# Optimization experiments

Measured on AMD Instinct MI355X. Metric: run time of the kernel, lower is better.

Reference implementation:

```python
import jax, jax.numpy as jnp
import numpy as np


def setup_inputs() -> dict:
    key = jax.random.key(0)
    k1, k2 = jax.random.split(key)
    # x: [B, D, H, W, C] 3D latent grid, C == embedding_dim
    x = jax.random.normal(k1, (4, 32, 32, 16, 256), dtype=jnp.float32)
    # codebook stored as (embedding_dim, num_embeddings) like the TF variable
    embeddings = jax.random.uniform(k2, (256, 4096), dtype=jnp.float32)
    return {"x": x, "embeddings": embeddings}


def reference(x, embeddings):
    # Inference-mode forward of VectorQuantizer.call (training=False).
    D, K = embeddings.shape  # (embedding_dim, num_embeddings)
    flat = x.reshape(-1, D)  # [N, D]
    # squared L2 distances: ||z||^2 + ||e||^2 - 2 z.e  -> [N, K]
    sim = flat @ embeddings
    dist = (jnp.sum(flat * flat, axis=1, keepdims=True)
            + jnp.sum(embeddings * embeddings, axis=0)
            - 2.0 * sim)
    idx = jnp.argmin(dist, axis=1)  # [N]
    # nearest-codebook lookup (gather codebook columns)
    quantized = jnp.take(embeddings.T, idx, axis=0).reshape(x.shape)
    # perplexity from code usage histogram (avoids materializing [N,K] one-hot)
    n = flat.shape[0]
    counts = jnp.zeros((K,), dtype=jnp.float32).at[idx].add(1.0)
    avg_probs = counts / n
    perplexity = jnp.exp(-jnp.sum(avg_probs * jnp.log(avg_probs + 1e-10)))
    return quantized, perplexity
```

## Files before the change

kernel.cpp:

```cpp
#include <hip/hip_runtime.h>
#include <hip/hip_bf16.h>

#define NROWS 65536
#define DIM   256
#define KCB   4096
#define CHUNK 32
#define NCH   (KCB / CHUNK)
#define NBUF  4
#define BUFB  16384
#define NENH_BASE (NBUF * BUFB)

typedef __attribute__((ext_vector_type(8))) short bf16x8;
typedef __attribute__((ext_vector_type(4))) float f32x4;

#define WAITV0 asm volatile("s_waitcnt vmcnt(0)" ::: "memory")
#define WAITV4 asm volatile("s_waitcnt vmcnt(4)" ::: "memory")
#define WAITV8 asm volatile("s_waitcnt vmcnt(8)" ::: "memory")

__device__ inline short f2bf(float f) {
    __hip_bfloat16 h = __float2bfloat16(f);
    return *reinterpret_cast<short*>(&h);
}

__global__ void prep_transpose(const float* __restrict__ E,
                               float* __restrict__ ET32,
                               ushort* __restrict__ ETbf)
{
    __shared__ float tile[64][65];
    const int kb = blockIdx.x * 64;
    const int db = blockIdx.y * 64;
    const int lo = threadIdx.x & 63;
    const int hi = threadIdx.x >> 6;

#pragma unroll
    for (int i = 0; i < 16; ++i) {
        int d = i * 4 + hi;
        tile[lo][d] = E[(size_t)(db + d) * KCB + kb + lo];
    }
    __syncthreads();
#pragma unroll
    for (int i = 0; i < 16; ++i) {
        int k = i * 4 + hi;
        float v = tile[k][lo];
        size_t off = (size_t)(kb + k) * DIM + db + lo;
        ET32[off] = v;
        ETbf[off] = (ushort)f2bf(v);
    }
}

__global__ void prep_enorm(const float* __restrict__ E, float* __restrict__ nenh)
{
    int k = blockIdx.x * 256 + threadIdx.x;
    float s = 0.0f;
#pragma unroll 8
    for (int d = 0; d < DIM; ++d) {
        float v = E[(size_t)d * KCB + k];
        s = fmaf(v, v, s);
    }
    nenh[k] = -0.5f * s;
}

__shared__ char lds_raw[NBUF * BUFB + 16384];

template <int BUF>
__device__ __forceinline__ void stage_chunk(
    const char* __restrict__ etb, const int (&soff)[4], int wave, int ct)
{
    const char* base = etb + (size_t)ct * (CHUNK * 512);
#pragma unroll
    for (int j = 0; j < 4; ++j) {
        __builtin_amdgcn_global_load_lds(
            (const __attribute__((address_space(1))) unsigned*)(base + soff[j]),
            (__attribute__((address_space(3))) unsigned*)
                (lds_raw + BUF * BUFB + wave * 4096 + j * 1024),
            16, 0, 0);
    }
}

template <int BUF, int TC>
__device__ __forceinline__ void read_batch(
    const int (&boffB)[8], int nhbyte, bf16x8 (&bfr)[8], float& nh)
{
#pragma unroll
    for (int kc = 0; kc < 8; ++kc)
        bfr[kc] = *(const bf16x8*)(lds_raw + BUF * BUFB + TC * 8192 + boffB[kc]);
    nh = *(const float*)(lds_raw + NENH_BASE + nhbyte);
}

__device__ __forceinline__ void mfma_cluster(
    const bf16x8 (&afrag)[2][8], const bf16x8 (&bfr)[8], float nh,
    float (&best)[2][4], int (&bidx)[2][4], int col)
{
    f32x4 acc0 = {nh, nh, nh, nh};
    f32x4 acc1 = {nh, nh, nh, nh};
    __builtin_amdgcn_s_setprio(1);
#pragma unroll
    for (int kc = 0; kc < 8; ++kc) {
        acc0 = __builtin_amdgcn_mfma_f32_16x16x32_bf16(afrag[0][kc], bfr[kc], acc0, 0, 0, 0);
        acc1 = __builtin_amdgcn_mfma_f32_16x16x32_bf16(afrag[1][kc], bfr[kc], acc1, 0, 0, 0);
    }
    __builtin_amdgcn_s_setprio(0);
#pragma unroll
    for (int r = 0; r < 4; ++r) {
        float s0 = acc0[r];
        bool g0 = s0 > best[0][r];
        bidx[0][r] = g0 ? col : bidx[0][r];
        best[0][r] = fmaxf(best[0][r], s0);
        float s1 = acc1[r];
        bool g1 = s1 > best[1][r];
        bidx[1][r] = g1 ? col : bidx[1][r];
        best[1][r] = fmaxf(best[1][r], s1);
    }
}

template <int BUF, int WN, bool STG, bool RA>
__device__ __forceinline__ void chunk_step(
    const char* __restrict__ etb, const int (&soff)[4], int wave, int ct,
    const int (&boffB)[8], int l15,
    const bf16x8 (&afrag)[2][8],
    bf16x8 (&bA)[8], bf16x8 (&bB)[8], float& nhA, float& nhB,
    float (&best)[2][4], int (&bidx)[2][4])
{
    if constexpr (WN == 4) { WAITV4; } else { WAITV0; }
    __builtin_amdgcn_s_barrier();
    __builtin_amdgcn_sched_barrier(0);
    if constexpr (STG) stage_chunk<(BUF + 3) & 3>(etb, soff, wave, ct + 3);
    read_batch<BUF, 1>(boffB, ct * 128 + 64 + l15 * 4, bB, nhB);
    mfma_cluster(afrag, bA, nhA, best, bidx, ct * CHUNK + l15);
    if constexpr (RA)
        read_batch<(BUF + 1) & 3, 0>(boffB, (ct + 1) * 128 + l15 * 4, bA, nhA);
    mfma_cluster(afrag, bB, nhB, best, bidx, ct * CHUNK + 16 + l15);
}

__global__ __launch_bounds__(256, 2)
void vq_argmin(const float* __restrict__ X,
               const ushort* __restrict__ ETbf,
               const float* __restrict__ nenh,
               int* __restrict__ idxout)
{
    const int tid  = threadIdx.x;
    const int lane = tid & 63;
    const int wave = tid >> 6;
    const int l15  = lane & 15;
    const int g    = lane >> 4;
    const int m    = l15 & 7;
    const long rowbase = (long)blockIdx.x * 128 + wave * 32;
    const char* etb = (const char*)ETbf;

    bf16x8 afrag[2][8];
#pragma unroll
    for (int rt = 0; rt < 2; ++rt) {
        const float* xr = X + (rowbase + rt * 16 + l15) * DIM;
#pragma unroll
        for (int kc = 0; kc < 8; ++kc) {
            int k0 = g * 64 + kc * 8;
            float4 v0 = *(const float4*)(xr + k0);
            float4 v1 = *(const float4*)(xr + k0 + 4);
            bf16x8 f;
            f[0] = f2bf(v0.x); f[1] = f2bf(v0.y);
            f[2] = f2bf(v0.z); f[3] = f2bf(v0.w);
            f[4] = f2bf(v1.x); f[5] = f2bf(v1.y);
            f[6] = f2bf(v1.z); f[7] = f2bf(v1.w);
            afrag[rt][kc] = f;
        }
    }

    int soff[4];
#pragma unroll
    for (int j = 0; j < 4; ++j) {
        const int o    = wave * 4096 + j * 1024 + lane * 16;
        const int col0 = o >> 9;
        const int cph  = (o >> 4) & 31;
        soff[j] = (col0 << 9) + ((cph ^ (col0 & 7)) << 4);
    }

    int boffB[8];
#pragma unroll
    for (int kc = 0; kc < 8; ++kc)
        boffB[kc] = l15 * 512 + ((((g << 3) + kc) ^ m) << 4);

#pragma unroll
    for (int j = 0; j < 4; ++j) {
        int o = wave * 4096 + j * 1024 + lane * 16;
        __builtin_amdgcn_global_load_lds(
            (const __attribute__((address_space(1))) unsigned*)((const char*)nenh + o),
            (__attribute__((address_space(3))) unsigned*)
                (lds_raw + NENH_BASE + wave * 4096 + j * 1024),
            16, 0, 0);
    }
    stage_chunk<0>(etb, soff, wave, 0);
    stage_chunk<1>(etb, soff, wave, 1);
    stage_chunk<2>(etb, soff, wave, 2);

    float best[2][4];
    int   bidx[2][4];
#pragma unroll
    for (int rt = 0; rt < 2; ++rt)
#pragma unroll
        for (int r = 0; r < 4; ++r) { best[rt][r] = -3.4e38f; bidx[rt][r] = 0x7fffffff; }

    bf16x8 bA[8], bB[8];
    float nhA, nhB;

    WAITV8;
    __builtin_amdgcn_s_barrier();
    __builtin_amdgcn_sched_barrier(0);
    read_batch<0, 0>(boffB, 0 + l15 * 4, bA, nhA);

    for (int gq = 0; gq < 31; ++gq) {
        const int ct = gq * 4;
        chunk_step<0, 4, true, true>(etb, soff, wave, ct + 0, boffB, l15,
                                     afrag, bA, bB, nhA, nhB, best, bidx);
        chunk_step<1, 4, true, true>(etb, soff, wave, ct + 1, boffB, l15,
                                     afrag, bA, bB, nhA, nhB, best, bidx);
        chunk_step<2, 4, true, true>(etb, soff, wave, ct + 2, boffB, l15,
                                     afrag, bA, bB, nhA, nhB, best, bidx);
        chunk_step<3, 4, true, true>(etb, soff, wave, ct + 3, boffB, l15,
                                     afrag, bA, bB, nhA, nhB, best, bidx);
    }
    chunk_step<0, 4, true,  true >(etb, soff, wave, 124, boffB, l15,
                                   afrag, bA, bB, nhA, nhB, best, bidx);
    chunk_step<1, 4, false, true >(etb, soff, wave, 125, boffB, l15,
                                   afrag, bA, bB, nhA, nhB, best, bidx);
    chunk_step<2, 0, false, true >(etb, soff, wave, 126, boffB, l15,
                                   afrag, bA, bB, nhA, nhB, best, bidx);
    chunk_step<3, 0, false, false>(etb, soff, wave, 127, boffB, l15,
                                   afrag, bA, bB, nhA, nhB, best, bidx);

#pragma unroll
    for (int rt = 0; rt < 2; ++rt) {
#pragma unroll
        for (int r = 0; r < 4; ++r) {
            float v = best[rt][r];
            int   ix = bidx[rt][r];
#pragma unroll
            for (int off = 1; off < 16; off <<= 1) {
                float ov = __shfl_xor(v, off, 64);
                int   oi = __shfl_xor(ix, off, 64);
                if (ov > v || (ov == v && oi < ix)) { v = ov; ix = oi; }
            }
            if (l15 == 0) {
                long row = rowbase + rt * 16 + g * 4 + r;
                idxout[row] = ix;
            }
        }
    }
}

__global__ void vq_gather(const int* __restrict__ idxin,
                          const float* __restrict__ ET32,
                          float* __restrict__ out,
                          unsigned* __restrict__ counts)
{
    const int tid = threadIdx.x;
    const long n  = (long)blockIdx.x * 4 + (tid >> 6);
    const int d4  = tid & 63;
    const int idx = idxin[n];
    float4 v = *(const float4*)(ET32 + (size_t)idx * DIM + d4 * 4);
    *(float4*)(out + n * DIM + d4 * 4) = v;
    if (d4 == 0) atomicAdd(&counts[idx], 1u);
}

__global__ void vq_perplexity(const unsigned* __restrict__ counts, float* __restrict__ outp)
{
    __shared__ float wsum[4];
    const int tid = threadIdx.x;
    float s = 0.0f;
    for (int k = tid; k < KCB; k += 256) {
        float p = (float)counts[k] * (1.0f / (float)NROWS);
        s += p * logf(p + 1e-10f);
    }
#pragma unroll
    for (int off = 32; off >= 1; off >>= 1) s += __shfl_down(s, off, 64);
    if ((tid & 63) == 0) wsum[tid >> 6] = s;
    __syncthreads();
    if (tid == 0) outp[0] = expf(-(wsum[0] + wsum[1] + wsum[2] + wsum[3]));
}

extern "C" void kernel_launch(void* const* d_in, const int* in_sizes, int n_in,
                              void* d_out, int out_size, void* d_ws, size_t ws_size,
                              hipStream_t stream)
{
    const float* X = (const float*)d_in[0];
    const float* E = (const float*)d_in[1];
    float* out = (float*)d_out;

    char* ws = (char*)d_ws;
    float*    ET32   = (float*)ws;
    ushort*   ETbf   = (ushort*)(ws + (size_t)KCB * DIM * 4);
    float*    nenh   = (float*)(ws + (size_t)KCB * DIM * 6);
    int*      idxbuf = (int*)(ws + (size_t)KCB * DIM * 6 + KCB * 4);
    unsigned* counts = (unsigned*)(ws + (size_t)KCB * DIM * 6 + KCB * 4 + NROWS * 4);

    hipMemsetAsync(counts, 0, KCB * sizeof(unsigned), stream);

    prep_transpose<<<dim3(KCB / 64, DIM / 64), dim3(256), 0, stream>>>(E, ET32, ETbf);
    prep_enorm<<<KCB / 256, dim3(256), 0, stream>>>(E, nenh);
    vq_argmin<<<NROWS / 128, dim3(256), 0, stream>>>(X, ETbf, nenh, idxbuf);
    vq_gather<<<NROWS / 4, dim3(256), 0, stream>>>(idxbuf, ET32, out, counts);
    vq_perplexity<<<1, dim3(256), 0, stream>>>(counts, out + (size_t)NROWS * DIM);
}
```

Before: 182.2 us.

## Use 2 waves per block with 64 rows each to double B-fragment reuse

Each block now has 2 waves instead of 4, and each wave owns 64 rows (4 row tiles) instead of 32. Every B fragment read from LDS therefore feeds 4 MFMAs instead of 2, which halves LDS reads per MFMA. Staging and nenh loads are widened to 8 per wave and the vmcnt waits are adjusted to match. The trade-off is more VGPR pressure (afrag, acc, best and bidx all double) and fewer waves per CU to hide latency.

Result: slower. 205.4 us (+12.8%).

```diff
diff --git a/kernel.cpp b/kernel.cpp
--- a/kernel.cpp
+++ b/kernel.cpp
@@ -13,9 +13,9 @@
 typedef __attribute__((ext_vector_type(8))) short bf16x8;
 typedef __attribute__((ext_vector_type(4))) float f32x4;
 
-#define WAITV0 asm volatile("s_waitcnt vmcnt(0)" ::: "memory")
-#define WAITV4 asm volatile("s_waitcnt vmcnt(4)" ::: "memory")
-#define WAITV8 asm volatile("s_waitcnt vmcnt(8)" ::: "memory")
+#define WAITV0  asm volatile("s_waitcnt vmcnt(0)" ::: "memory")
+#define WAITV8  asm volatile("s_waitcnt vmcnt(8)" ::: "memory")
+#define WAITV16 asm volatile("s_waitcnt vmcnt(16)" ::: "memory")
 
 __device__ inline short f2bf(float f) {
     __hip_bfloat16 h = __float2bfloat16(f);
@@ -64,15 +64,15 @@
 
 template <int BUF>
 __device__ __forceinline__ void stage_chunk(
-    const char* __restrict__ etb, const int (&soff)[4], int wave, int ct)
+    const char* __restrict__ etb, const int (&soff)[8], int wave, int ct)
 {
     const char* base = etb + (size_t)ct * (CHUNK * 512);
 #pragma unroll
-    for (int j = 0; j < 4; ++j) {
+    for (int j = 0; j < 8; ++j) {
         __builtin_amdgcn_global_load_lds(
             (const __attribute__((address_space(1))) unsigned*)(base + soff[j]),
             (__attribute__((address_space(3))) unsigned*)
-                (lds_raw + BUF * BUFB + wave * 4096 + j * 1024),
+                (lds_raw + BUF * BUFB + wave * 8192 + j * 1024),
             16, 0, 0);
     }
 }
@@ -88,40 +88,40 @@
 }
 
 __device__ __forceinline__ void mfma_cluster(
-    const bf16x8 (&afrag)[2][8], const bf16x8 (&bfr)[8], float nh,
-    float (&best)[2][4], int (&bidx)[2][4], int col)
-{
-    f32x4 acc0 = {nh, nh, nh, nh};
-    f32x4 acc1 = {nh, nh, nh, nh};
+    const bf16x8 (&afrag)[4][8], const bf16x8 (&bfr)[8], float nh,
+    float (&best)[4][4], int (&bidx)[4][4], int col)
+{
+    f32x4 acc[4];
+#pragma unroll
+    for (int rt = 0; rt < 4; ++rt) acc[rt] = {nh, nh, nh, nh};
     __builtin_amdgcn_s_setprio(1);
 #pragma unroll
-    for (int kc = 0; kc < 8; ++kc) {
-        acc0 = __builtin_amdgcn_mfma_f32_16x16x32_bf16(afrag[0][kc], bfr[kc], acc0, 0, 0, 0);
-        acc1 = __builtin_amdgcn_mfma_f32_16x16x32_bf16(afrag[1][kc], bfr[kc], acc1, 0, 0, 0);
-    }
+    for (int kc = 0; kc < 8; ++kc)
+#pragma unroll
+        for (int rt = 0; rt < 4; ++rt)
+            acc[rt] = __builtin_amdgcn_mfma_f32_16x16x32_bf16(
+                afrag[rt][kc], bfr[kc], acc[rt], 0, 0, 0);
     __builtin_amdgcn_s_setprio(0);
 #pragma unroll
-    for (int r = 0; r < 4; ++r) {
-        float s0 = acc0[r];
-        bool g0 = s0 > best[0][r];
-        bidx[0][r] = g0 ? col : bidx[0][r];
-        best[0][r] = fmaxf(best[0][r], s0);
-        float s1 = acc1[r];
-        bool g1 = s1 > best[1][r];
-        bidx[1][r] = g1 ? col : bidx[1][r];
-        best[1][r] = fmaxf(best[1][r], s1);
-    }
+    for (int rt = 0; rt < 4; ++rt)
+#pragma unroll
+        for (int r = 0; r < 4; ++r) {
+            float s = acc[rt][r];
+            bool gt = s > best[rt][r];
+            bidx[rt][r] = gt ? col : bidx[rt][r];
+            best[rt][r] = fmaxf(best[rt][r], s);
+        }
 }
 
 template <int BUF, int WN, bool STG, bool RA>
 __device__ __forceinline__ void chunk_step(
-    const char* __restrict__ etb, const int (&soff)[4], int wave, int ct,
+    const char* __restrict__ etb, const int (&soff)[8], int wave, int ct,
     const int (&boffB)[8], int l15,
-    const bf16x8 (&afrag)[2][8],
+    const bf16x8 (&afrag)[4][8],
     bf16x8 (&bA)[8], bf16x8 (&bB)[8], float& nhA, float& nhB,
-    float (&best)[2][4], int (&bidx)[2][4])
-{
-    if constexpr (WN == 4) { WAITV4; } else { WAITV0; }
+    float (&best)[4][4], int (&bidx)[4][4])
+{
+    if constexpr (WN == 8) { WAITV8; } else { WAITV0; }
     __builtin_amdgcn_s_barrier();
     __builtin_amdgcn_sched_barrier(0);
     if constexpr (STG) stage_chunk<(BUF + 3) & 3>(etb, soff, wave, ct + 3);
@@ -132,7 +132,7 @@
     mfma_cluster(afrag, bB, nhB, best, bidx, ct * CHUNK + 16 + l15);
 }
 
-__global__ __launch_bounds__(256, 2)
+__global__ __launch_bounds__(128, 1)
 void vq_argmin(const float* __restrict__ X,
                const ushort* __restrict__ ETbf,
                const float* __restrict__ nenh,
@@ -144,12 +144,12 @@
     const int l15  = lane & 15;
     const int g    = lane >> 4;
     const int m    = l15 & 7;
-    const long rowbase = (long)blockIdx.x * 128 + wave * 32;
+    const long rowbase = (long)blockIdx.x * 128 + wave * 64;
     const char* etb = (const char*)ETbf;
 
-    bf16x8 afrag[2][8];
-#pragma unroll
-    for (int rt = 0; rt < 2; ++rt) {
+    bf16x8 afrag[4][8];
+#pragma unroll
+    for (int rt = 0; rt < 4; ++rt) {
         const float* xr = X + (rowbase + rt * 16 + l15) * DIM;
 #pragma unroll
         for (int kc = 0; kc < 8; ++kc) {
@@ -165,10 +165,10 @@
         }
     }
 
-    int soff[4];
-#pragma unroll
-    for (int j = 0; j < 4; ++j) {
-        const int o    = wave * 4096 + j * 1024 + lane * 16;
+    int soff[8];
+#pragma unroll
+    for (int j = 0; j < 8; ++j) {
+        const int o    = wave * 8192 + j * 1024 + lane * 16;
         const int col0 = o >> 9;
         const int cph  = (o >> 4) & 31;
         soff[j] = (col0 << 9) + ((cph ^ (col0 & 7)) << 4);
@@ -180,47 +180,47 @@
         boffB[kc] = l15 * 512 + ((((g << 3) + kc) ^ m) << 4);
 
 #pragma unroll
-    for (int j = 0; j < 4; ++j) {
-        int o = wave * 4096 + j * 1024 + lane * 16;
+    for (int j = 0; j < 8; ++j) {
+        int o = wave * 8192 + j * 1024 + lane * 16;
         __builtin_amdgcn_global_load_lds(
             (const __attribute__((address_space(1))) unsigned*)((const char*)nenh + o),
             (__attribute__((address_space(3))) unsigned*)
-                (lds_raw + NENH_BASE + wave * 4096 + j * 1024),
+                (lds_raw + NENH_BASE + wave * 8192 + j * 1024),
             16, 0, 0);
     }
     stage_chunk<0>(etb, soff, wave, 0);
     stage_chunk<1>(etb, soff, wave, 1);
     stage_chunk<2>(etb, soff, wave, 2);
 
-    float best[2][4];
-    int   bidx[2][4];
-#pragma unroll
-    for (int rt = 0; rt < 2; ++rt)
+    float best[4][4];
+    int   bidx[4][4];
+#pragma unroll
+    for (int rt = 0; rt < 4; ++rt)
 #pragma unroll
         for (int r = 0; r < 4; ++r) { best[rt][r] = -3.4e38f; bidx[rt][r] = 0x7fffffff; }
 
     bf16x8 bA[8], bB[8];
     float nhA, nhB;
 
-    WAITV8;
+    WAITV16;
     __builtin_amdgcn_s_barrier();
     __builtin_amdgcn_sched_barrier(0);
     read_batch<0, 0>(boffB, 0 + l15 * 4, bA, nhA);
 
     for (int gq = 0; gq < 31; ++gq) {
         const int ct = gq * 4;
-        chunk_step<0, 4, true, true>(etb, soff, wave, ct + 0, boffB, l15,
+        chunk_step<0, 8, true, true>(etb, soff, wave, ct + 0, boffB, l15,
                                      afrag, bA, bB, nhA, nhB, best, bidx);
-        chunk_step<1, 4, true, true>(etb, soff, wave, ct + 1, boffB, l15,
+        chunk_step<1, 8, true, true>(etb, soff, wave, ct + 1, boffB, l15,
                                      afrag, bA, bB, nhA, nhB, best, bidx);
-        chunk_step<2, 4, true, true>(etb, soff, wave, ct + 2, boffB, l15,
+        chunk_step<2, 8, true, true>(etb, soff, wave, ct + 2, boffB, l15,
                                      afrag, bA, bB, nhA, nhB, best, bidx);
-        chunk_step<3, 4, true, true>(etb, soff, wave, ct + 3, boffB, l15,
+        chunk_step<3, 8, true, true>(etb, soff, wave, ct + 3, boffB, l15,
                                      afrag, bA, bB, nhA, nhB, best, bidx);
     }
-    chunk_step<0, 4, true,  true >(etb, soff, wave, 124, boffB, l15,
+    chunk_step<0, 8, true,  true >(etb, soff, wave, 124, boffB, l15,
                                    afrag, bA, bB, nhA, nhB, best, bidx);
-    chunk_step<1, 4, false, true >(etb, soff, wave, 125, boffB, l15,
+    chunk_step<1, 8, false, true >(etb, soff, wave, 125, boffB, l15,
                                    afrag, bA, bB, nhA, nhB, best, bidx);
     chunk_step<2, 0, false, true >(etb, soff, wave, 126, boffB, l15,
                                    afrag, bA, bB, nhA, nhB, best, bidx);
@@ -228,7 +228,7 @@
                                    afrag, bA, bB, nhA, nhB, best, bidx);
 
 #pragma unroll
-    for (int rt = 0; rt < 2; ++rt) {
+    for (int rt = 0; rt < 4; ++rt) {
 #pragma unroll
         for (int r = 0; r < 4; ++r) {
             float v = best[rt][r];
@@ -296,7 +296,7 @@
 
     prep_transpose<<<dim3(KCB / 64, DIM / 64), dim3(256), 0, stream>>>(E, ET32, ETbf);
     prep_enorm<<<KCB / 256, dim3(256), 0, stream>>>(E, nenh);
-    vq_argmin<<<NROWS / 128, dim3(256), 0, stream>>>(X, ETbf, nenh, idxbuf);
+    vq_argmin<<<NROWS / 128, dim3(128), 0, stream>>>(X, ETbf, nenh, idxbuf);
     vq_gather<<<NROWS / 4, dim3(256), 0, stream>>>(idxbuf, ET32, out, counts);
     vq_perplexity<<<1, dim3(256), 0, stream>>>(counts, out + (size_t)NROWS * DIM);
 }
```
